# Optimization experiments

Hardware: AMD Instinct MI355X
Metric: run time of the kernel (lower is better)

Reference implementation:

```python
import jax, jax.numpy as jnp
import numpy as np

B, S, H, FF, E = 4, 4096, 1024, 4096, 8
EPS = 1e-5


def setup_inputs() -> dict:
    key = jax.random.key(0)
    ks = jax.random.split(key, 8)
    std = 0.02
    return {
        "x": jax.random.normal(ks[0], (B, S, H), jnp.float32),
        "norm_weight": jnp.ones((H,), jnp.float32),
        "router_w": jax.random.normal(ks[1], (E, H), jnp.float32) * std,
        "router_b": jnp.zeros((E,), jnp.float32),
        "fc1_w": jax.random.normal(ks[2], (E, FF, H), jnp.float32) * std,
        "fc1_b": jnp.zeros((E, FF), jnp.float32),
        "fc2_w": jax.random.normal(ks[3], (E, H, FF), jnp.float32) * std,
        "fc2_b": jnp.zeros((E, H), jnp.float32),
    }


def reference(x, norm_weight, router_w, router_b, fc1_w, fc1_b, fc2_w, fc2_b):
    b, s, h = x.shape
    T = b * s
    e = router_w.shape[0]
    cap = T // e  # expert capacity, capacity_factor = 1.0

    x_flat = x.reshape(T, h)
    # RMSNorm (pre-norm on MoE input)
    xn = x_flat * jax.lax.rsqrt(jnp.mean(x_flat * x_flat, axis=-1, keepdims=True) + EPS) * norm_weight

    # Router (no jitter: eval / jitter_noise=0)
    logits = xn @ router_w.T + router_b          # [T, E]
    probs = jax.nn.softmax(logits, axis=-1)       # [T, E]

    # Expert-choice routing: each expert picks its top-`cap` tokens by prob
    gates, idx = jax.lax.top_k(probs.T, cap)      # [E, cap], [E, cap]

    # Dispatch (gather) and grouped expert MLP
    xe = xn[idx]                                   # [E, cap, H]
    hmid = jnp.einsum('ech,efh->ecf', xe, fc1_w) + fc1_b[:, None, :]
    hmid = jax.nn.gelu(hmid, approximate=False)    # torch F.gelu default (exact)
    ye = jnp.einsum('ecf,ehf->ech', hmid, fc2_w) + fc2_b[:, None, :]

    # Combine: gated scatter-add back to token positions, normalize by gate sum
    flat_idx = idx.reshape(-1)                     # [E*cap]
    weighted = (ye * gates[..., None]).reshape(-1, h)
    out = jnp.zeros((T, h), x.dtype).at[flat_idx].add(weighted)
    gate_sums = jnp.zeros((T, 1), x.dtype).at[flat_idx].add(gates.reshape(-1, 1))
    out = out / jnp.maximum(gate_sums, 1e-9)       # unrouted tokens stay zero
    return out.reshape(b, s, h)
```

## Files before the change

kernel.cpp:

```cpp
#include <hip/hip_runtime.h>
#include <hip/hip_bf16.h>

#define T_TOK 16384
#define H_DIM 1024
#define FF_DIM 4096
#define NE 8
#define CAP 2048
#define EPS_F 1e-5f

#define BM2 256
#define BN2 256
#define BK64 64

typedef __attribute__((ext_vector_type(4))) float f32x4;
typedef __attribute__((ext_vector_type(8))) short bf16x8;
typedef unsigned long long u64;
typedef unsigned int u32;

__device__ inline void gload_lds16(const void* g, void* l) {
  __builtin_amdgcn_global_load_lds(
      (const __attribute__((address_space(1))) unsigned int*)g,
      (__attribute__((address_space(3))) unsigned int*)l, 16, 0, 0);
}

__device__ inline unsigned short bf16_bits(float f) {
  __hip_bfloat16 h = __float2bfloat16(f);
  unsigned short u;
  __builtin_memcpy(&u, &h, 2);
  return u;
}

__device__ inline float bits_f32(unsigned short u) {
  const u32 x = ((u32)u) << 16;
  float f;
  __builtin_memcpy(&f, &x, 4);
  return f;
}

__global__ __launch_bounds__(256) void router_kernel(
    const float* __restrict__ x, const float* __restrict__ nw,
    const float* __restrict__ rw, const float* __restrict__ rb,
    __hip_bfloat16* __restrict__ xn, u64* __restrict__ keys) {
  const int t = blockIdx.x;
  const int tid = threadIdx.x;
  const float4 v = reinterpret_cast<const float4*>(x + (size_t)t * H_DIM)[tid];
  float ss = v.x * v.x + v.y * v.y + v.z * v.z + v.w * v.w;
#pragma unroll
  for (int o = 32; o > 0; o >>= 1) ss += __shfl_down(ss, o);
  __shared__ float red[4];
  __shared__ float redl[4][NE];
  const int wv = tid >> 6, ln = tid & 63;
  if (ln == 0) red[wv] = ss;
  __syncthreads();
  const float tot = red[0] + red[1] + red[2] + red[3];
  const float scale = rsqrtf(tot * (1.0f / H_DIM) + EPS_F);
  const float4 w4 = reinterpret_cast<const float4*>(nw)[tid];
  float xv0 = v.x * scale * w4.x, xv1 = v.y * scale * w4.y;
  float xv2 = v.z * scale * w4.z, xv3 = v.w * scale * w4.w;
  ushort4 u4;
  u4.x = bf16_bits(xv0); u4.y = bf16_bits(xv1);
  u4.z = bf16_bits(xv2); u4.w = bf16_bits(xv3);
  reinterpret_cast<ushort4*>(xn + (size_t)t * H_DIM)[tid] = u4;
  float lg[NE];
#pragma unroll
  for (int e = 0; e < NE; ++e) {
    const float4 r4 = reinterpret_cast<const float4*>(rw + (size_t)e * H_DIM)[tid];
    lg[e] = xv0 * r4.x + xv1 * r4.y + xv2 * r4.z + xv3 * r4.w;
  }
#pragma unroll
  for (int o = 32; o > 0; o >>= 1) {
#pragma unroll
    for (int e = 0; e < NE; ++e) lg[e] += __shfl_down(lg[e], o);
  }
  if (ln == 0) {
#pragma unroll
    for (int e = 0; e < NE; ++e) redl[wv][e] = lg[e];
  }
  __syncthreads();
  if (tid == 0) {
    float l[NE];
    float m = -1e30f;
#pragma unroll
    for (int e = 0; e < NE; ++e) {
      l[e] = redl[0][e] + redl[1][e] + redl[2][e] + redl[3][e] + rb[e];
      m = fmaxf(m, l[e]);
    }
    float s = 0.f;
#pragma unroll
    for (int e = 0; e < NE; ++e) { l[e] = expf(l[e] - m); s += l[e]; }
    const float inv = 1.0f / s;
#pragma unroll
    for (int e = 0; e < NE; ++e) {
      const float p = l[e] * inv;
      const u64 key = ((u64)__float_as_uint(p) << 32) | (u32)(0xFFFFFFFFu - (u32)t);
      keys[(size_t)e * T_TOK + t] = key;
    }
  }
}

#define EQCAP 7168
__global__ __launch_bounds__(1024) void topk_kernel(
    const u64* __restrict__ keys, int* __restrict__ idxl,
    float* __restrict__ gatel, int* __restrict__ tok_list, int* __restrict__ tok_cnt) {
  const int e = blockIdx.x;
  const int tid = threadIdx.x;
  const int lane = tid & 63;
  const u64* ke = keys + (size_t)e * T_TOK;
  __shared__ int hist[256];
  __shared__ u32 s_pref;
  __shared__ int s_k;
  __shared__ int s_cnt;
  __shared__ int s_eq;
  __shared__ u32 eqlist[EQCAP];

  u32 pref = 0;
  int pbits = 0;
  int kneed = CAP;
  for (int pass = 0; pass < 4; ++pass) {
    if (tid < 256) hist[tid] = 0;
    __syncthreads();
    const int shift = 24 - 8 * pass;
    for (int i = tid; i < T_TOK; i += 1024) {
      const u32 hi = (u32)(ke[i] >> 32);
      const bool ok = (pbits == 0) || ((hi >> (32 - pbits)) == pref);
      const int d = ok ? (int)((hi >> shift) & 255) : -1;
      u64 act = __ballot(ok);
      while (act) {
        const int src = __ffsll((long long)act) - 1;
        const int dl = __shfl(d, src);
        const u64 mb = __ballot(ok && (d == dl));
        if (lane == src) atomicAdd(&hist[dl], (int)__popcll(mb));
        act &= ~mb;
      }
    }
    __syncthreads();
    if (tid == 0) {
      int cum = 0;
      int d = 255;
      for (; d >= 0; --d) {
        cum += hist[d];
        if (cum >= kneed) break;
      }
      s_k = kneed - (cum - hist[d]);
      s_pref = (pref << 8) | (u32)d;
    }
    __syncthreads();
    pref = s_pref;
    kneed = s_k;
    pbits += 8;
    __syncthreads();
  }
  const u32 thrp = pref;
  const float thrp_f = __uint_as_float(thrp);

  if (tid == 0) { s_cnt = 0; s_eq = 0; }
  __syncthreads();
  for (int i = tid; i < T_TOK; i += 1024) {
    const u64 key = ke[i];
    const u32 hi = (u32)(key >> 32);
    if (hi > thrp) {
      const int pos = atomicAdd(&s_cnt, 1);
      if (pos < CAP) {
        const int tok = (int)(0xFFFFFFFFu - (u32)key);
        idxl[e * CAP + pos] = tok;
        gatel[e * CAP + pos] = __uint_as_float(hi);
        const int j = atomicAdd(tok_cnt + tok, 1);
        if (j < NE) tok_list[tok * NE + j] = e * CAP + pos;
      }
    } else if (hi == thrp) {
      const int j = atomicAdd(&s_eq, 1);
      if (j < EQCAP) eqlist[j] = (u32)key;
    }
  }
  __syncthreads();
  const int neq = s_eq;
  if (neq <= EQCAP) {
    u32 prefl = 0;
    int pb = 0;
    int kn = kneed;
    if (neq > kneed) {
      for (int pass = 0; pass < 4; ++pass) {
        if (tid < 256) hist[tid] = 0;
        __syncthreads();
        const int shift = 24 - 8 * pass;
        for (int i = tid; i < neq; i += 1024) {
          const u32 vv = eqlist[i];
          if ((pb == 0) || ((vv >> (32 - pb)) == prefl)) atomicAdd(&hist[(vv >> shift) & 255], 1);
        }
        __syncthreads();
        if (tid == 0) {
          int cum = 0;
          int d = 255;
          for (; d >= 0; --d) {
            cum += hist[d];
            if (cum >= kn) break;
          }
          s_k = kn - (cum - hist[d]);
          s_pref = (prefl << 8) | (u32)d;
        }
        __syncthreads();
        prefl = s_pref;
        kn = s_k;
        pb += 8;
        __syncthreads();
      }
    }
    for (int i = tid; i < neq; i += 1024) {
      const u32 lo = eqlist[i];
      if (neq <= kneed || lo >= prefl) {
        const int pos = atomicAdd(&s_cnt, 1);
        if (pos < CAP) {
          const int tok = (int)(0xFFFFFFFFu - lo);
          idxl[e * CAP + pos] = tok;
          gatel[e * CAP + pos] = thrp_f;
          const int j = atomicAdd(tok_cnt + tok, 1);
          if (j < NE) tok_list[tok * NE + j] = e * CAP + pos;
        }
      }
    }
  } else {
    u64 pref64 = (u64)thrp;
    int pb64 = 32;
    int kn = kneed;
    for (int pass = 4; pass < 8; ++pass) {
      if (tid < 256) hist[tid] = 0;
      __syncthreads();
      const int shift = 56 - 8 * pass;
      for (int i = tid; i < T_TOK; i += 1024) {
        const u64 key = ke[i];
        if ((key >> (64 - pb64)) == pref64) atomicAdd(&hist[(int)((key >> shift) & 255)], 1);
      }
      __syncthreads();
      if (tid == 0) {
        int cum = 0;
        int d = 255;
        for (; d >= 0; --d) {
          cum += hist[d];
          if (cum >= kn) break;
        }
        s_k = kn - (cum - hist[d]);
        s_pref = (u32)d;
      }
      __syncthreads();
      pref64 = (pref64 << 8) | s_pref;
      kn = s_k;
      pb64 += 8;
      __syncthreads();
    }
    for (int i = tid; i < T_TOK; i += 1024) {
      const u64 key = ke[i];
      if ((u32)(key >> 32) == thrp && key >= pref64) {
        const int pos = atomicAdd(&s_cnt, 1);
        if (pos < CAP) {
          const int tok = (int)(0xFFFFFFFFu - (u32)key);
          idxl[e * CAP + pos] = tok;
          gatel[e * CAP + pos] = thrp_f;
          const int j = atomicAdd(tok_cnt + tok, 1);
          if (j < NE) tok_list[tok * NE + j] = e * CAP + pos;
        }
      }
    }
  }
}

__global__ __launch_bounds__(256) void cvt2_kernel(
    const float* __restrict__ s1, __hip_bfloat16* __restrict__ d1,
    const float* __restrict__ s2, __hip_bfloat16* __restrict__ d2, int n4each) {
  int i = blockIdx.x * blockDim.x + threadIdx.x;
  const int stride = gridDim.x * blockDim.x;
  for (; i < 2 * n4each; i += stride) {
    const float* s = (i < n4each) ? s1 : s2;
    __hip_bfloat16* d = (i < n4each) ? d1 : d2;
    const int j = (i < n4each) ? i : i - n4each;
    const float4 v = reinterpret_cast<const float4*>(s)[j];
    ushort4 o;
    o.x = bf16_bits(v.x); o.y = bf16_bits(v.y);
    o.z = bf16_bits(v.z); o.w = bf16_bits(v.w);
    reinterpret_cast<ushort4*>(d)[j] = o;
  }
}

template <int MODE>
__global__ __launch_bounds__(1024, 4) void gemm8_kernel(
    const __hip_bfloat16* __restrict__ Asrc, const __hip_bfloat16* __restrict__ Bw,
    const float* __restrict__ bias, const int* __restrict__ idxl,
    const float* __restrict__ gatel, __hip_bfloat16* __restrict__ hmid,
    __hip_bfloat16* __restrict__ ye, int ebase) {
  constexpr int N = (MODE == 0) ? FF_DIM : H_DIM;
  constexpr int K = (MODE == 0) ? H_DIM : FF_DIM;
  constexpr int NBN = N / BN2;
  constexpr int LOG_NBN = (MODE == 0) ? 4 : 2;
  constexpr int BPE = (CAP / BM2) * NBN;
  constexpr int LOG_BPE = (MODE == 0) ? 7 : 5;
  constexpr int NT = K / BK64;

  const int nwg = gridDim.x;
  const int wg0 = blockIdx.x;
  const int wg = (wg0 & 7) * (nwg >> 3) + (wg0 >> 3);
  const int z = wg >> LOG_BPE;
  const int rr = wg & (BPE - 1);
  const int bm = rr >> LOG_NBN;
  const int bn = rr & (NBN - 1);
  const int e = ebase + z;

  const int tid = threadIdx.x;
  const int lane = tid & 63;
  const int w = tid >> 6;
  const int wr = w >> 2, wc = w & 3;
  const int fr = lane & 15, q = lane >> 4;

  __shared__ char smem[131072];

  const int srow = tid >> 3;
  const int sg = tid & 7;
  const int skoff = (sg ^ (srow & 7)) * 8;

  const __hip_bfloat16* asrc0;
  const __hip_bfloat16* asrc1;
  if constexpr (MODE == 0) {
    const int t0 = idxl[e * CAP + bm * BM2 + srow];
    const int t1 = idxl[e * CAP + bm * BM2 + 128 + srow];
    asrc0 = Asrc + (size_t)t0 * H_DIM + skoff;
    asrc1 = Asrc + (size_t)t1 * H_DIM + skoff;
  } else {
    asrc0 = Asrc + ((size_t)z * CAP + bm * BM2 + srow) * FF_DIM + skoff;
    asrc1 = asrc0 + (size_t)128 * FF_DIM;
  }
  const __hip_bfloat16* bsrc0 = Bw + (size_t)z * N * K + (size_t)(bn * BN2 + srow) * K + skoff;
  const __hip_bfloat16* bsrc1 = bsrc0 + (size_t)128 * K;

  int aoffs[4][2], boffs[4][2];
#pragma unroll
  for (int m = 0; m < 4; ++m) {
    const int row = wr * 64 + m * 16 + fr;
#pragma unroll
    for (int ks = 0; ks < 2; ++ks)
      aoffs[m][ks] = row * 128 + (((ks * 4 + q) ^ (row & 7)) << 4);
  }
#pragma unroll
  for (int n = 0; n < 4; ++n) {
    const int row = wc * 64 + n * 16 + fr;
#pragma unroll
    for (int ks = 0; ks < 2; ++ks)
      boffs[n][ks] = 32768 + row * 128 + (((ks * 4 + q) ^ (row & 7)) << 4);
  }

  f32x4 acc[4][4] = {};
  bf16x8 Af[4], Bf[4];

#define STAGE8(sb, k0)                                       \
  do {                                                       \
    char* d_ = smem + (sb)*65536 + tid * 16;                 \
    gload_lds16(asrc0 + (k0), d_);                           \
    gload_lds16(asrc1 + (k0), d_ + 16384);                   \
    gload_lds16(bsrc0 + (k0), d_ + 32768);                   \
    gload_lds16(bsrc1 + (k0), d_ + 49152);                   \
  } while (0)

  STAGE8(0, 0);
  asm volatile("s_waitcnt vmcnt(0)");
  __builtin_amdgcn_s_barrier();
  __builtin_amdgcn_sched_barrier(0);

  for (int kt = 0; kt < NT; ++kt) {
    const char* base = smem + (kt & 1) * 65536;
    if (kt + 1 < NT) STAGE8((kt + 1) & 1, (kt + 1) * BK64);
    Af[0] = *reinterpret_cast<const bf16x8*>(base + aoffs[0][0]);
    Af[1] = *reinterpret_cast<const bf16x8*>(base + aoffs[1][0]);
    Af[2] = *reinterpret_cast<const bf16x8*>(base + aoffs[2][0]);
    Af[3] = *reinterpret_cast<const bf16x8*>(base + aoffs[3][0]);
    Bf[0] = *reinterpret_cast<const bf16x8*>(base + boffs[0][0]);
    Bf[1] = *reinterpret_cast<const bf16x8*>(base + boffs[1][0]);
    Bf[2] = *reinterpret_cast<const bf16x8*>(base + boffs[2][0]);
    Bf[3] = *reinterpret_cast<const bf16x8*>(base + boffs[3][0]);
    asm volatile("s_waitcnt lgkmcnt(0)");
    __builtin_amdgcn_sched_barrier(0);
    __builtin_amdgcn_s_setprio(1);
#pragma unroll
    for (int m_ = 0; m_ < 4; ++m_)
#pragma unroll
      for (int n_ = 0; n_ < 4; ++n_)
        acc[m_][n_] = __builtin_amdgcn_mfma_f32_16x16x32_bf16(Af[m_], Bf[n_], acc[m_][n_], 0, 0, 0);
    __builtin_amdgcn_s_setprio(0);
    Af[0] = *reinterpret_cast<const bf16x8*>(base + aoffs[0][1]);
    Af[1] = *reinterpret_cast<const bf16x8*>(base + aoffs[1][1]);
    Af[2] = *reinterpret_cast<const bf16x8*>(base + aoffs[2][1]);
    Af[3] = *reinterpret_cast<const bf16x8*>(base + aoffs[3][1]);
    Bf[0] = *reinterpret_cast<const bf16x8*>(base + boffs[0][1]);
    Bf[1] = *reinterpret_cast<const bf16x8*>(base + boffs[1][1]);
    Bf[2] = *reinterpret_cast<const bf16x8*>(base + boffs[2][1]);
    Bf[3] = *reinterpret_cast<const bf16x8*>(base + boffs[3][1]);
    asm volatile("s_waitcnt lgkmcnt(0)");
    __builtin_amdgcn_sched_barrier(0);
    __builtin_amdgcn_s_setprio(1);
#pragma unroll
    for (int m_ = 0; m_ < 4; ++m_)
#pragma unroll
      for (int n_ = 0; n_ < 4; ++n_)
        acc[m_][n_] = __builtin_amdgcn_mfma_f32_16x16x32_bf16(Af[m_], Bf[n_], acc[m_][n_], 0, 0, 0);
    __builtin_amdgcn_s_setprio(0);
    asm volatile("s_waitcnt vmcnt(0)");
    __builtin_amdgcn_s_barrier();
    __builtin_amdgcn_sched_barrier(0);
  }
#undef STAGE8

  if constexpr (MODE == 0) {
#pragma unroll
    for (int m = 0; m < 4; ++m) {
      const int rbase = bm * BM2 + wr * 64 + m * 16 + q * 4;
#pragma unroll
      for (int n = 0; n < 4; ++n) {
        const int gn = bn * BN2 + wc * 64 + n * 16 + fr;
        const float bb = bias[e * FF_DIM + gn];
#pragma unroll
        for (int i = 0; i < 4; ++i) {
          const float v = acc[m][n][i] + bb;
          const float u = v * (1.5957691216f + 0.0713548162972f * v * v);
          const float s = 1.0f / (1.0f + __expf(-u));
          hmid[((size_t)z * CAP + rbase + i) * FF_DIM + gn] = __float2bfloat16(v * s);
        }
      }
    }
  } else {
#pragma unroll
    for (int m = 0; m < 4; ++m) {
      const int rbase = bm * BM2 + wr * 64 + m * 16 + q * 4;
      float gt[4];
#pragma unroll
      for (int i = 0; i < 4; ++i) gt[i] = gatel[e * CAP + rbase + i];
#pragma unroll
      for (int n = 0; n < 4; ++n) {
        const int gn = bn * BN2 + wc * 64 + n * 16 + fr;
        const float bb = bias[e * H_DIM + gn];
#pragma unroll
        for (int i = 0; i < 4; ++i)
          ye[((size_t)e * CAP + rbase + i) * H_DIM + gn] =
              __float2bfloat16((acc[m][n][i] + bb) * gt[i]);
      }
    }
  }
}

__global__ __launch_bounds__(256) void combine_kernel(
    const __hip_bfloat16* __restrict__ ye, const float* __restrict__ gatel,
    const int* __restrict__ tok_list, const int* __restrict__ tok_cnt,
    float* __restrict__ out) {
  const int t = blockIdx.x;
  const int tid = threadIdx.x;
  const int cnt = tok_cnt[t];
  float a0 = 0.f, a1 = 0.f, a2 = 0.f, a3 = 0.f, gs = 0.f;
  for (int j = 0; j < cnt && j < NE; ++j) {
    const int ent = tok_list[t * NE + j];
    gs += gatel[ent];
    const ushort4 v = reinterpret_cast<const ushort4*>(ye + (size_t)ent * H_DIM)[tid];
    a0 += bits_f32(v.x);
    a1 += bits_f32(v.y);
    a2 += bits_f32(v.z);
    a3 += bits_f32(v.w);
  }
  const float inv = 1.0f / fmaxf(gs, 1e-9f);
  float4 o;
  o.x = a0 * inv; o.y = a1 * inv; o.z = a2 * inv; o.w = a3 * inv;
  reinterpret_cast<float4*>(out + (size_t)t * H_DIM)[tid] = o;
}

extern "C" void kernel_launch(void* const* d_in, const int* in_sizes, int n_in,
                              void* d_out, int out_size, void* d_ws, size_t ws_size,
                              hipStream_t stream) {
  const float* x = (const float*)d_in[0];
  const float* nw = (const float*)d_in[1];
  const float* rw = (const float*)d_in[2];
  const float* rb = (const float*)d_in[3];
  const float* fc1w = (const float*)d_in[4];
  const float* fc1b = (const float*)d_in[5];
  const float* fc2w = (const float*)d_in[6];
  const float* fc2b = (const float*)d_in[7];
  float* out = (float*)d_out;

  char* ws = (char*)d_ws;
  size_t off = 0;
  auto alloc = [&](size_t b) {
    char* p = ws + off;
    off += (b + 255) & ~(size_t)255;
    return p;
  };
  __hip_bfloat16* xn = (__hip_bfloat16*)alloc((size_t)T_TOK * H_DIM * 2);
  u64* keys = (u64*)alloc((size_t)NE * T_TOK * 8);
  int* idxl = (int*)alloc((size_t)NE * CAP * 4);
  float* gatel = (float*)alloc((size_t)NE * CAP * 4);
  int* tok_list = (int*)alloc((size_t)T_TOK * NE * 4);
  int* tok_cnt = (int*)alloc((size_t)T_TOK * 4);
  __hip_bfloat16* ye = (__hip_bfloat16*)alloc((size_t)NE * CAP * H_DIM * 2);

  int EC = NE;
  while (EC > 1) {
    const size_t per = (size_t)EC * ((size_t)FF_DIM * H_DIM * 2 * 2 + (size_t)CAP * FF_DIM * 2);
    if (off + per + 4096 <= ws_size) break;
    EC >>= 1;
  }
  __hip_bfloat16* w1b = (__hip_bfloat16*)alloc((size_t)EC * FF_DIM * H_DIM * 2);
  __hip_bfloat16* w2b = (__hip_bfloat16*)alloc((size_t)EC * H_DIM * FF_DIM * 2);
  __hip_bfloat16* hmid = (__hip_bfloat16*)alloc((size_t)EC * CAP * FF_DIM * 2);

  hipMemsetAsync(tok_cnt, 0, (size_t)T_TOK * 4, stream);

  router_kernel<<<T_TOK, 256, 0, stream>>>(x, nw, rw, rb, xn, keys);
  topk_kernel<<<NE, 1024, 0, stream>>>(keys, idxl, gatel, tok_list, tok_cnt);

  for (int eb = 0; eb < NE; eb += EC) {
    const int n4 = EC * FF_DIM * H_DIM / 4;
    cvt2_kernel<<<4096, 256, 0, stream>>>(fc1w + (size_t)eb * FF_DIM * H_DIM, w1b,
                                          fc2w + (size_t)eb * H_DIM * FF_DIM, w2b, n4);
    const int nb1 = EC * (CAP / BM2) * (FF_DIM / BN2);
    gemm8_kernel<0><<<nb1, 1024, 0, stream>>>(xn, w1b, fc1b, idxl, gatel, hmid, ye, eb);
    const int nb2 = EC * (CAP / BM2) * (H_DIM / BN2);
    gemm8_kernel<1><<<nb2, 1024, 0, stream>>>(hmid, w2b, fc2b, idxl, gatel, hmid, ye, eb);
  }
  combine_kernel<<<T_TOK, 256, 0, stream>>>(ye, gatel, tok_list, tok_cnt, out);
}
```

Measured before the change: 533.7 us.

## Fuse fp32 weight conversion into expert GEMMs with triple-buffered K=32 pipeline

Drops the separate kernel that converted fc1/fc2 weights to bf16. The GEMM kernels now stream fp32 weights straight into LDS and convert them to bf16 while loading fragments. The K loop moves from double buffering with BK=64 to a three-stage ring with BK=32 and a 3-stage prefetch depth. This saves a full read and write of the weights and one launch, but doubles the weight bytes each GEMM tile reads from global memory and LDS, and adds conversion ALU work inside the main loop.

```diff
diff --git a/kernel.cpp b/kernel.cpp
--- a/kernel.cpp
+++ b/kernel.cpp
@@ -10,7 +10,7 @@
 
 #define BM2 256
 #define BN2 256
-#define BK64 64
+#define BK2 32
 
 typedef __attribute__((ext_vector_type(4))) float f32x4;
 typedef __attribute__((ext_vector_type(8))) short bf16x8;
@@ -263,26 +263,9 @@
   }
 }
 
-__global__ __launch_bounds__(256) void cvt2_kernel(
-    const float* __restrict__ s1, __hip_bfloat16* __restrict__ d1,
-    const float* __restrict__ s2, __hip_bfloat16* __restrict__ d2, int n4each) {
-  int i = blockIdx.x * blockDim.x + threadIdx.x;
-  const int stride = gridDim.x * blockDim.x;
-  for (; i < 2 * n4each; i += stride) {
-    const float* s = (i < n4each) ? s1 : s2;
-    __hip_bfloat16* d = (i < n4each) ? d1 : d2;
-    const int j = (i < n4each) ? i : i - n4each;
-    const float4 v = reinterpret_cast<const float4*>(s)[j];
-    ushort4 o;
-    o.x = bf16_bits(v.x); o.y = bf16_bits(v.y);
-    o.z = bf16_bits(v.z); o.w = bf16_bits(v.w);
-    reinterpret_cast<ushort4*>(d)[j] = o;
-  }
-}
-
 template <int MODE>
-__global__ __launch_bounds__(1024, 4) void gemm8_kernel(
-    const __hip_bfloat16* __restrict__ Asrc, const __hip_bfloat16* __restrict__ Bw,
+__global__ __launch_bounds__(1024, 4) void gemm9_kernel(
+    const __hip_bfloat16* __restrict__ Asrc, const float* __restrict__ Bw,
     const float* __restrict__ bias, const int* __restrict__ idxl,
     const float* __restrict__ gatel, __hip_bfloat16* __restrict__ hmid,
     __hip_bfloat16* __restrict__ ye, int ebase) {
@@ -292,7 +275,7 @@
   constexpr int LOG_NBN = (MODE == 0) ? 4 : 2;
   constexpr int BPE = (CAP / BM2) * NBN;
   constexpr int LOG_BPE = (MODE == 0) ? 7 : 5;
-  constexpr int NT = K / BK64;
+  constexpr int NT = K / BK2;
 
   const int nwg = gridDim.x;
   const int wg0 = blockIdx.x;
@@ -309,71 +292,69 @@
   const int wr = w >> 2, wc = w & 3;
   const int fr = lane & 15, q = lane >> 4;
 
-  __shared__ char smem[131072];
-
-  const int srow = tid >> 3;
-  const int sg = tid & 7;
-  const int skoff = (sg ^ (srow & 7)) * 8;
-
-  const __hip_bfloat16* asrc0;
-  const __hip_bfloat16* asrc1;
+  __shared__ char smem[147456];
+
+  const int arow = tid >> 2;
+  const int ag = tid & 3;
+  const int askz = (ag ^ ((arow >> 1) & 3)) * 8;
+  const __hip_bfloat16* asrc;
   if constexpr (MODE == 0) {
-    const int t0 = idxl[e * CAP + bm * BM2 + srow];
-    const int t1 = idxl[e * CAP + bm * BM2 + 128 + srow];
-    asrc0 = Asrc + (size_t)t0 * H_DIM + skoff;
-    asrc1 = Asrc + (size_t)t1 * H_DIM + skoff;
+    const int t0 = idxl[e * CAP + bm * BM2 + arow];
+    asrc = Asrc + (size_t)t0 * H_DIM + askz;
   } else {
-    asrc0 = Asrc + ((size_t)z * CAP + bm * BM2 + srow) * FF_DIM + skoff;
-    asrc1 = asrc0 + (size_t)128 * FF_DIM;
-  }
-  const __hip_bfloat16* bsrc0 = Bw + (size_t)z * N * K + (size_t)(bn * BN2 + srow) * K + skoff;
-  const __hip_bfloat16* bsrc1 = bsrc0 + (size_t)128 * K;
-
-  int aoffs[4][2], boffs[4][2];
-#pragma unroll
-  for (int m = 0; m < 4; ++m) {
-    const int row = wr * 64 + m * 16 + fr;
-#pragma unroll
-    for (int ks = 0; ks < 2; ++ks)
-      aoffs[m][ks] = row * 128 + (((ks * 4 + q) ^ (row & 7)) << 4);
-  }
-#pragma unroll
-  for (int n = 0; n < 4; ++n) {
-    const int row = wc * 64 + n * 16 + fr;
-#pragma unroll
-    for (int ks = 0; ks < 2; ++ks)
-      boffs[n][ks] = 32768 + row * 128 + (((ks * 4 + q) ^ (row & 7)) << 4);
-  }
+    asrc = Asrc + ((size_t)z * CAP + bm * BM2 + arow) * FF_DIM + askz;
+  }
+  const int brow = tid >> 3;
+  const int bg = tid & 7;
+  const int bskz = (bg ^ (brow & 7)) * 4;
+  const float* bsrc0 = Bw + (size_t)z * N * K + (size_t)(bn * BN2 + brow) * K + bskz;
+  const float* bsrc1 = bsrc0 + (size_t)128 * K;
 
   f32x4 acc[4][4] = {};
-  bf16x8 Af[4], Bf[4];
-
-#define STAGE8(sb, k0)                                       \
-  do {                                                       \
-    char* d_ = smem + (sb)*65536 + tid * 16;                 \
-    gload_lds16(asrc0 + (k0), d_);                           \
-    gload_lds16(asrc1 + (k0), d_ + 16384);                   \
-    gload_lds16(bsrc0 + (k0), d_ + 32768);                   \
-    gload_lds16(bsrc1 + (k0), d_ + 49152);                   \
+
+#define STAGE9(sb, k0)                                   \
+  do {                                                   \
+    char* d_ = smem + (sb)*49152 + tid * 16;             \
+    gload_lds16(asrc + (k0), d_);                        \
+    gload_lds16(bsrc0 + (k0), d_ + 16384);               \
+    gload_lds16(bsrc1 + (k0), d_ + 32768);               \
   } while (0)
 
-  STAGE8(0, 0);
-  asm volatile("s_waitcnt vmcnt(0)");
+  STAGE9(0, 0);
+  STAGE9(1, BK2);
+  STAGE9(2, 2 * BK2);
+  asm volatile("s_waitcnt vmcnt(6)");
   __builtin_amdgcn_s_barrier();
   __builtin_amdgcn_sched_barrier(0);
 
   for (int kt = 0; kt < NT; ++kt) {
-    const char* base = smem + (kt & 1) * 65536;
-    if (kt + 1 < NT) STAGE8((kt + 1) & 1, (kt + 1) * BK64);
-    Af[0] = *reinterpret_cast<const bf16x8*>(base + aoffs[0][0]);
-    Af[1] = *reinterpret_cast<const bf16x8*>(base + aoffs[1][0]);
-    Af[2] = *reinterpret_cast<const bf16x8*>(base + aoffs[2][0]);
-    Af[3] = *reinterpret_cast<const bf16x8*>(base + aoffs[3][0]);
-    Bf[0] = *reinterpret_cast<const bf16x8*>(base + boffs[0][0]);
-    Bf[1] = *reinterpret_cast<const bf16x8*>(base + boffs[1][0]);
-    Bf[2] = *reinterpret_cast<const bf16x8*>(base + boffs[2][0]);
-    Bf[3] = *reinterpret_cast<const bf16x8*>(base + boffs[3][0]);
+    const int sl = kt % 3;
+    const char* base = smem + sl * 49152;
+    bf16x8 Af[4], Bf[4];
+#pragma unroll
+    for (int m = 0; m < 4; ++m)
+      Af[m] = *reinterpret_cast<const bf16x8*>(
+          base + (wr * 64 + m * 16 + fr) * 64 + ((q ^ ((fr >> 1) & 3)) << 4));
+#pragma unroll
+    for (int n = 0; n < 4; ++n) {
+      const int row = wc * 64 + n * 16 + fr;
+      const char* rb = base + 16384 + row * 128;
+      const float4 lo = *reinterpret_cast<const float4*>(rb + (((2 * q) ^ (row & 7)) << 4));
+      const float4 hi = *reinterpret_cast<const float4*>(rb + (((2 * q + 1) ^ (row & 7)) << 4));
+      bf16x8 f;
+      f[0] = (short)bf16_bits(lo.x); f[1] = (short)bf16_bits(lo.y);
+      f[2] = (short)bf16_bits(lo.z); f[3] = (short)bf16_bits(lo.w);
+      f[4] = (short)bf16_bits(hi.x); f[5] = (short)bf16_bits(hi.y);
+      f[6] = (short)bf16_bits(hi.z); f[7] = (short)bf16_bits(hi.w);
+      Bf[n] = f;
+    }
     asm volatile("s_waitcnt lgkmcnt(0)");
+    __builtin_amdgcn_sched_barrier(0);
+    __builtin_amdgcn_s_barrier();
+    __builtin_amdgcn_sched_barrier(0);
+    const int kref = (kt + 3 < NT) ? (kt + 3) : (kt + 3 - NT);
+    STAGE9(sl, kref * BK2);
+    asm volatile("s_waitcnt vmcnt(6)");
     __builtin_amdgcn_sched_barrier(0);
     __builtin_amdgcn_s_setprio(1);
 #pragma unroll
@@ -382,28 +363,10 @@
       for (int n_ = 0; n_ < 4; ++n_)
         acc[m_][n_] = __builtin_amdgcn_mfma_f32_16x16x32_bf16(Af[m_], Bf[n_], acc[m_][n_], 0, 0, 0);
     __builtin_amdgcn_s_setprio(0);
-    Af[0] = *reinterpret_cast<const bf16x8*>(base + aoffs[0][1]);
-    Af[1] = *reinterpret_cast<const bf16x8*>(base + aoffs[1][1]);
-    Af[2] = *reinterpret_cast<const bf16x8*>(base + aoffs[2][1]);
-    Af[3] = *reinterpret_cast<const bf16x8*>(base + aoffs[3][1]);
-    Bf[0] = *reinterpret_cast<const bf16x8*>(base + boffs[0][1]);
-    Bf[1] = *reinterpret_cast<const bf16x8*>(base + boffs[1][1]);
-    Bf[2] = *reinterpret_cast<const bf16x8*>(base + boffs[2][1]);
-    Bf[3] = *reinterpret_cast<const bf16x8*>(base + boffs[3][1]);
-    asm volatile("s_waitcnt lgkmcnt(0)");
-    __builtin_amdgcn_sched_barrier(0);
-    __builtin_amdgcn_s_setprio(1);
-#pragma unroll
-    for (int m_ = 0; m_ < 4; ++m_)
-#pragma unroll
-      for (int n_ = 0; n_ < 4; ++n_)
-        acc[m_][n_] = __builtin_amdgcn_mfma_f32_16x16x32_bf16(Af[m_], Bf[n_], acc[m_][n_], 0, 0, 0);
-    __builtin_amdgcn_s_setprio(0);
-    asm volatile("s_waitcnt vmcnt(0)");
     __builtin_amdgcn_s_barrier();
     __builtin_amdgcn_sched_barrier(0);
   }
-#undef STAGE8
+#undef STAGE9
 
   if constexpr (MODE == 0) {
 #pragma unroll
@@ -495,12 +458,10 @@
 
   int EC = NE;
   while (EC > 1) {
-    const size_t per = (size_t)EC * ((size_t)FF_DIM * H_DIM * 2 * 2 + (size_t)CAP * FF_DIM * 2);
+    const size_t per = (size_t)EC * (size_t)CAP * FF_DIM * 2;
     if (off + per + 4096 <= ws_size) break;
     EC >>= 1;
   }
-  __hip_bfloat16* w1b = (__hip_bfloat16*)alloc((size_t)EC * FF_DIM * H_DIM * 2);
-  __hip_bfloat16* w2b = (__hip_bfloat16*)alloc((size_t)EC * H_DIM * FF_DIM * 2);
   __hip_bfloat16* hmid = (__hip_bfloat16*)alloc((size_t)EC * CAP * FF_DIM * 2);
 
   hipMemsetAsync(tok_cnt, 0, (size_t)T_TOK * 4, stream);
@@ -509,13 +470,12 @@
   topk_kernel<<<NE, 1024, 0, stream>>>(keys, idxl, gatel, tok_list, tok_cnt);
 
   for (int eb = 0; eb < NE; eb += EC) {
-    const int n4 = EC * FF_DIM * H_DIM / 4;
-    cvt2_kernel<<<4096, 256, 0, stream>>>(fc1w + (size_t)eb * FF_DIM * H_DIM, w1b,
-                                          fc2w + (size_t)eb * H_DIM * FF_DIM, w2b, n4);
     const int nb1 = EC * (CAP / BM2) * (FF_DIM / BN2);
-    gemm8_kernel<0><<<nb1, 1024, 0, stream>>>(xn, w1b, fc1b, idxl, gatel, hmid, ye, eb);
+    gemm9_kernel<0><<<nb1, 1024, 0, stream>>>(xn, fc1w + (size_t)eb * FF_DIM * H_DIM, fc1b,
+                                              idxl, gatel, hmid, ye, eb);
     const int nb2 = EC * (CAP / BM2) * (H_DIM / BN2);
-    gemm8_kernel<1><<<nb2, 1024, 0, stream>>>(hmid, w2b, fc2b, idxl, gatel, hmid, ye, eb);
+    gemm9_kernel<1><<<nb2, 1024, 0, stream>>>(hmid, fc2w + (size_t)eb * H_DIM * FF_DIM, fc2b,
+                                              idxl, gatel, hmid, ye, eb);
   }
   combine_kernel<<<T_TOK, 256, 0, stream>>>(ye, gatel, tok_list, tok_cnt, out);
 }
```

Measured after the change: 629.7 us. +18.0%, slower.

## Use 4-stage BK=32 LDS pipeline in expert GEMMs and fuse weight cast into router

Applied to the files above, without the earlier changes.

The expert GEMM main loop moves from a double-buffered BK=64 schedule to a four-slot BK=32 ring with three tiles in flight. A and B global-to-LDS loads are split across the two MFMA half-steps, and each iteration uses finer waitcnt and barriers, aiming to hide more memory latency. The fp32-to-bf16 weight conversion and the tok_cnt zeroing move into the router kernel, removing the cvt2 launch and the memset when all experts fit in the workspace. The risks are more barriers per unit of K, a changed LDS swizzle, and a router kernel that now does heavy grid-stride conversion work per block.

```diff
diff --git a/kernel.cpp b/kernel.cpp
--- a/kernel.cpp
+++ b/kernel.cpp
@@ -10,7 +10,7 @@
 
 #define BM2 256
 #define BN2 256
-#define BK64 64
+#define BK2 32
 
 typedef __attribute__((ext_vector_type(4))) float f32x4;
 typedef __attribute__((ext_vector_type(8))) short bf16x8;
@@ -40,9 +40,13 @@
 __global__ __launch_bounds__(256) void router_kernel(
     const float* __restrict__ x, const float* __restrict__ nw,
     const float* __restrict__ rw, const float* __restrict__ rb,
-    __hip_bfloat16* __restrict__ xn, u64* __restrict__ keys) {
+    __hip_bfloat16* __restrict__ xn, u64* __restrict__ keys,
+    int* __restrict__ tok_cnt,
+    const float* __restrict__ w1s, __hip_bfloat16* __restrict__ w1d,
+    const float* __restrict__ w2s, __hip_bfloat16* __restrict__ w2d, int do_cvt) {
   const int t = blockIdx.x;
   const int tid = threadIdx.x;
+  if (tid == 0) tok_cnt[t] = 0;
   const float4 v = reinterpret_cast<const float4*>(x + (size_t)t * H_DIM)[tid];
   float ss = v.x * v.x + v.y * v.y + v.z * v.z + v.w * v.w;
 #pragma unroll
@@ -94,6 +98,20 @@
       const float p = l[e] * inv;
       const u64 key = ((u64)__float_as_uint(p) << 32) | (u32)(0xFFFFFFFFu - (u32)t);
       keys[(size_t)e * T_TOK + t] = key;
+    }
+  }
+  if (do_cvt) {
+    const int n4each = NE * FF_DIM * H_DIM / 4;
+    const int gstride = gridDim.x * blockDim.x;
+    for (int i = blockIdx.x * blockDim.x + tid; i < 2 * n4each; i += gstride) {
+      const float* s = (i < n4each) ? w1s : w2s;
+      __hip_bfloat16* d = (i < n4each) ? w1d : w2d;
+      const int j = (i < n4each) ? i : i - n4each;
+      const float4 vv = reinterpret_cast<const float4*>(s)[j];
+      ushort4 o;
+      o.x = bf16_bits(vv.x); o.y = bf16_bits(vv.y);
+      o.z = bf16_bits(vv.z); o.w = bf16_bits(vv.w);
+      reinterpret_cast<ushort4*>(d)[j] = o;
     }
   }
 }
@@ -281,7 +299,7 @@
 }
 
 template <int MODE>
-__global__ __launch_bounds__(1024, 4) void gemm8_kernel(
+__global__ __launch_bounds__(1024) void gemm7_kernel(
     const __hip_bfloat16* __restrict__ Asrc, const __hip_bfloat16* __restrict__ Bw,
     const float* __restrict__ bias, const int* __restrict__ idxl,
     const float* __restrict__ gatel, __hip_bfloat16* __restrict__ hmid,
@@ -292,7 +310,7 @@
   constexpr int LOG_NBN = (MODE == 0) ? 4 : 2;
   constexpr int BPE = (CAP / BM2) * NBN;
   constexpr int LOG_BPE = (MODE == 0) ? 7 : 5;
-  constexpr int NT = K / BK64;
+  constexpr int NT = K / BK2;
 
   const int nwg = gridDim.x;
   const int wg0 = blockIdx.x;
@@ -311,99 +329,82 @@
 
   __shared__ char smem[131072];
 
-  const int srow = tid >> 3;
-  const int sg = tid & 7;
-  const int skoff = (sg ^ (srow & 7)) * 8;
-
-  const __hip_bfloat16* asrc0;
-  const __hip_bfloat16* asrc1;
+  const int srow = tid >> 2;
+  const int sg = tid & 3;
+  const int skoff = (sg ^ ((srow >> 1) & 3)) * 8;
+
+  const __hip_bfloat16* asrc;
   if constexpr (MODE == 0) {
     const int t0 = idxl[e * CAP + bm * BM2 + srow];
-    const int t1 = idxl[e * CAP + bm * BM2 + 128 + srow];
-    asrc0 = Asrc + (size_t)t0 * H_DIM + skoff;
-    asrc1 = Asrc + (size_t)t1 * H_DIM + skoff;
+    asrc = Asrc + (size_t)t0 * H_DIM + skoff;
   } else {
-    asrc0 = Asrc + ((size_t)z * CAP + bm * BM2 + srow) * FF_DIM + skoff;
-    asrc1 = asrc0 + (size_t)128 * FF_DIM;
-  }
-  const __hip_bfloat16* bsrc0 = Bw + (size_t)z * N * K + (size_t)(bn * BN2 + srow) * K + skoff;
-  const __hip_bfloat16* bsrc1 = bsrc0 + (size_t)128 * K;
-
-  int aoffs[4][2], boffs[4][2];
-#pragma unroll
-  for (int m = 0; m < 4; ++m) {
-    const int row = wr * 64 + m * 16 + fr;
-#pragma unroll
-    for (int ks = 0; ks < 2; ++ks)
-      aoffs[m][ks] = row * 128 + (((ks * 4 + q) ^ (row & 7)) << 4);
-  }
-#pragma unroll
-  for (int n = 0; n < 4; ++n) {
-    const int row = wc * 64 + n * 16 + fr;
-#pragma unroll
-    for (int ks = 0; ks < 2; ++ks)
-      boffs[n][ks] = 32768 + row * 128 + (((ks * 4 + q) ^ (row & 7)) << 4);
-  }
+    asrc = Asrc + ((size_t)z * CAP + bm * BM2 + srow) * FF_DIM + skoff;
+  }
+  const __hip_bfloat16* bsrc = Bw + (size_t)z * N * K + (size_t)(bn * BN2 + srow) * K + skoff;
+
+  const int slotk = ((q ^ ((fr >> 1) & 3)) << 4);
+  const int aoff0 = (wr * 64 + fr) * 64 + slotk;
+  const int boff0 = 16384 + (wc * 64 + fr) * 64 + slotk;
 
   f32x4 acc[4][4] = {};
   bf16x8 Af[4], Bf[4];
 
-#define STAGE8(sb, k0)                                       \
-  do {                                                       \
-    char* d_ = smem + (sb)*65536 + tid * 16;                 \
-    gload_lds16(asrc0 + (k0), d_);                           \
-    gload_lds16(asrc1 + (k0), d_ + 16384);                   \
-    gload_lds16(bsrc0 + (k0), d_ + 32768);                   \
-    gload_lds16(bsrc1 + (k0), d_ + 49152);                   \
-  } while (0)
-
-  STAGE8(0, 0);
-  asm volatile("s_waitcnt vmcnt(0)");
+#define GLDA(sb, k0) gload_lds16(asrc + (k0), smem + (sb)*32768 + tid * 16)
+#define GLDB(sb, k0) gload_lds16(bsrc + (k0), smem + (sb)*32768 + 16384 + tid * 16)
+
+  GLDA(0, 0); GLDB(0, 0);
+  GLDA(1, BK2); GLDB(1, BK2);
+  GLDA(2, 2 * BK2); GLDB(2, 2 * BK2);
+  asm volatile("s_waitcnt vmcnt(4)");
   __builtin_amdgcn_s_barrier();
   __builtin_amdgcn_sched_barrier(0);
 
   for (int kt = 0; kt < NT; ++kt) {
-    const char* base = smem + (kt & 1) * 65536;
-    if (kt + 1 < NT) STAGE8((kt + 1) & 1, (kt + 1) * BK64);
-    Af[0] = *reinterpret_cast<const bf16x8*>(base + aoffs[0][0]);
-    Af[1] = *reinterpret_cast<const bf16x8*>(base + aoffs[1][0]);
-    Af[2] = *reinterpret_cast<const bf16x8*>(base + aoffs[2][0]);
-    Af[3] = *reinterpret_cast<const bf16x8*>(base + aoffs[3][0]);
-    Bf[0] = *reinterpret_cast<const bf16x8*>(base + boffs[0][0]);
-    Bf[1] = *reinterpret_cast<const bf16x8*>(base + boffs[1][0]);
-    Bf[2] = *reinterpret_cast<const bf16x8*>(base + boffs[2][0]);
-    Bf[3] = *reinterpret_cast<const bf16x8*>(base + boffs[3][0]);
+    const int cur = kt & 3;
+    const int kref = (kt + 3 < NT) ? (kt + 3) : (kt + 3 - NT);
+    const int k0p = kref * BK2;
+    const int psl = (kt + 3) & 3;
+    const char* base = smem + cur * 32768;
+
+    Af[0] = *reinterpret_cast<const bf16x8*>(base + aoff0);
+    Af[1] = *reinterpret_cast<const bf16x8*>(base + aoff0 + 1024);
+    Af[2] = *reinterpret_cast<const bf16x8*>(base + aoff0 + 2048);
+    Af[3] = *reinterpret_cast<const bf16x8*>(base + aoff0 + 3072);
+    Bf[0] = *reinterpret_cast<const bf16x8*>(base + boff0);
+    Bf[1] = *reinterpret_cast<const bf16x8*>(base + boff0 + 1024);
+    __builtin_amdgcn_sched_barrier(0);
+    Bf[2] = *reinterpret_cast<const bf16x8*>(base + boff0 + 2048);
+    Bf[3] = *reinterpret_cast<const bf16x8*>(base + boff0 + 3072);
+    GLDA(psl, k0p);
+    asm volatile("s_waitcnt vmcnt(3)");
+    __builtin_amdgcn_s_barrier();
+    asm volatile("s_waitcnt lgkmcnt(2)");
+    __builtin_amdgcn_sched_barrier(0);
+    __builtin_amdgcn_s_setprio(1);
+#pragma unroll
+    for (int m_ = 0; m_ < 4; ++m_) {
+      acc[m_][0] = __builtin_amdgcn_mfma_f32_16x16x32_bf16(Af[m_], Bf[0], acc[m_][0], 0, 0, 0);
+      acc[m_][1] = __builtin_amdgcn_mfma_f32_16x16x32_bf16(Af[m_], Bf[1], acc[m_][1], 0, 0, 0);
+    }
+    __builtin_amdgcn_s_setprio(0);
+    __builtin_amdgcn_sched_barrier(0);
+
+    GLDB(psl, k0p);
     asm volatile("s_waitcnt lgkmcnt(0)");
     __builtin_amdgcn_sched_barrier(0);
-    __builtin_amdgcn_s_setprio(1);
-#pragma unroll
-    for (int m_ = 0; m_ < 4; ++m_)
-#pragma unroll
-      for (int n_ = 0; n_ < 4; ++n_)
-        acc[m_][n_] = __builtin_amdgcn_mfma_f32_16x16x32_bf16(Af[m_], Bf[n_], acc[m_][n_], 0, 0, 0);
-    __builtin_amdgcn_s_setprio(0);
-    Af[0] = *reinterpret_cast<const bf16x8*>(base + aoffs[0][1]);
-    Af[1] = *reinterpret_cast<const bf16x8*>(base + aoffs[1][1]);
-    Af[2] = *reinterpret_cast<const bf16x8*>(base + aoffs[2][1]);
-    Af[3] = *reinterpret_cast<const bf16x8*>(base + aoffs[3][1]);
-    Bf[0] = *reinterpret_cast<const bf16x8*>(base + boffs[0][1]);
-    Bf[1] = *reinterpret_cast<const bf16x8*>(base + boffs[1][1]);
-    Bf[2] = *reinterpret_cast<const bf16x8*>(base + boffs[2][1]);
-    Bf[3] = *reinterpret_cast<const bf16x8*>(base + boffs[3][1]);
-    asm volatile("s_waitcnt lgkmcnt(0)");
+    __builtin_amdgcn_s_barrier();
     __builtin_amdgcn_sched_barrier(0);
     __builtin_amdgcn_s_setprio(1);
 #pragma unroll
-    for (int m_ = 0; m_ < 4; ++m_)
-#pragma unroll
-      for (int n_ = 0; n_ < 4; ++n_)
-        acc[m_][n_] = __builtin_amdgcn_mfma_f32_16x16x32_bf16(Af[m_], Bf[n_], acc[m_][n_], 0, 0, 0);
+    for (int m_ = 0; m_ < 4; ++m_) {
+      acc[m_][2] = __builtin_amdgcn_mfma_f32_16x16x32_bf16(Af[m_], Bf[2], acc[m_][2], 0, 0, 0);
+      acc[m_][3] = __builtin_amdgcn_mfma_f32_16x16x32_bf16(Af[m_], Bf[3], acc[m_][3], 0, 0, 0);
+    }
     __builtin_amdgcn_s_setprio(0);
-    asm volatile("s_waitcnt vmcnt(0)");
-    __builtin_amdgcn_s_barrier();
     __builtin_amdgcn_sched_barrier(0);
   }
-#undef STAGE8
+#undef GLDA
+#undef GLDB
 
   if constexpr (MODE == 0) {
 #pragma unroll
@@ -503,19 +504,22 @@
   __hip_bfloat16* w2b = (__hip_bfloat16*)alloc((size_t)EC * H_DIM * FF_DIM * 2);
   __hip_bfloat16* hmid = (__hip_bfloat16*)alloc((size_t)EC * CAP * FF_DIM * 2);
 
-  hipMemsetAsync(tok_cnt, 0, (size_t)T_TOK * 4, stream);
-
-  router_kernel<<<T_TOK, 256, 0, stream>>>(x, nw, rw, rb, xn, keys);
+  const int fused_cvt = (EC == NE) ? 1 : 0;
+
+  router_kernel<<<T_TOK, 256, 0, stream>>>(x, nw, rw, rb, xn, keys, tok_cnt,
+                                           fc1w, w1b, fc2w, w2b, fused_cvt);
   topk_kernel<<<NE, 1024, 0, stream>>>(keys, idxl, gatel, tok_list, tok_cnt);
 
   for (int eb = 0; eb < NE; eb += EC) {
-    const int n4 = EC * FF_DIM * H_DIM / 4;
-    cvt2_kernel<<<4096, 256, 0, stream>>>(fc1w + (size_t)eb * FF_DIM * H_DIM, w1b,
-                                          fc2w + (size_t)eb * H_DIM * FF_DIM, w2b, n4);
+    if (!fused_cvt) {
+      const int n4 = EC * FF_DIM * H_DIM / 4;
+      cvt2_kernel<<<4096, 256, 0, stream>>>(fc1w + (size_t)eb * FF_DIM * H_DIM, w1b,
+                                            fc2w + (size_t)eb * H_DIM * FF_DIM, w2b, n4);
+    }
     const int nb1 = EC * (CAP / BM2) * (FF_DIM / BN2);
-    gemm8_kernel<0><<<nb1, 1024, 0, stream>>>(xn, w1b, fc1b, idxl, gatel, hmid, ye, eb);
+    gemm7_kernel<0><<<nb1, 1024, 0, stream>>>(xn, w1b, fc1b, idxl, gatel, hmid, ye, eb);
     const int nb2 = EC * (CAP / BM2) * (H_DIM / BN2);
-    gemm8_kernel<1><<<nb2, 1024, 0, stream>>>(hmid, w2b, fc2b, idxl, gatel, hmid, ye, eb);
+    gemm7_kernel<1><<<nb2, 1024, 0, stream>>>(hmid, w2b, fc2b, idxl, gatel, hmid, ye, eb);
   }
   combine_kernel<<<T_TOK, 256, 0, stream>>>(ye, gatel, tok_list, tok_cnt, out);
 }
```

New measurement: 505.3 us, median of 3. 1.06x faster.
